# Kernel tuning notes

Hardware: AMD Instinct MI355X
Metric: run time of the kernel (lower is better)

Reference implementation:

```python
import jax, jax.numpy as jnp
import numpy as np

N_NODES = 50000
N_EDGES = 1_600_000
IN_DIM = 128
HID = 32
HEADS = 4
NEG_SLOPE = 0.2


def setup_inputs() -> dict:
    key = jax.random.key(0)
    ks = jax.random.split(key, 6)
    h = jax.random.normal(ks[0], (N_NODES, IN_DIM), dtype=jnp.float32)
    src = jax.random.randint(ks[1], (N_EDGES,), 0, N_NODES, dtype=jnp.int32)
    dst = jax.random.randint(ks[2], (N_EDGES,), 0, N_NODES, dtype=jnp.int32)
    s = 1.0 / np.sqrt(IN_DIM)  # ~ Linear default init scale
    Wq = (jax.random.normal(ks[3], (HEADS, IN_DIM, HID), dtype=jnp.float32) * s)
    Wk = (jax.random.normal(ks[4], (HEADS, IN_DIM, HID), dtype=jnp.float32) * s)
    Wv = (jax.random.normal(ks[5], (HEADS, IN_DIM, HID), dtype=jnp.float32) * s)
    return {"h": h, "src": src, "dst": dst, "Wq": Wq, "Wk": Wk, "Wv": Wv}


def _gat_forward(h, src, dst, Wq, Wk, Wv):
    n = h.shape[0]
    # per-head projections: [H, N, D]
    q = jnp.einsum('ni,hio->hno', h, Wq)
    k = jnp.einsum('ni,hio->hno', h, Wk)
    v = jnp.einsum('ni,hio->hno', h, Wv)
    # edge scores: e = leaky_relu(<q_src, k_dst>)  -> [H, E]
    e = jax.nn.leaky_relu(jnp.einsum('hed,hed->he', q[:, src], k[:, dst]),
                          negative_slope=NEG_SLOPE)
    # segment softmax over incoming edges of each dst node
    seg_max = jax.vmap(lambda x: jax.ops.segment_max(x, dst, num_segments=n))(e)
    seg_max = jax.lax.stop_gradient(jnp.where(jnp.isfinite(seg_max), seg_max, 0.0))
    ex = jnp.exp(e - seg_max[:, dst])                       # [H, E]
    denom = jax.vmap(lambda x: jax.ops.segment_sum(x, dst, num_segments=n))(ex)
    alpha = ex / jnp.maximum(denom, 1e-9)[:, dst]           # [H, E]
    # weighted scatter-sum of source values into dst nodes: [H, N, D]
    msg = alpha[..., None] * v[:, src]
    out = jax.vmap(lambda m: jax.ops.segment_sum(m, dst, num_segments=n))(msg)
    # concat heads along feature dim -> [N, H*D]
    return out.transpose(1, 0, 2).reshape(n, HEADS * HID)


def reference(h, src, dst, Wq, Wk, Wv):
    return _gat_forward(h, src, dst, Wq, Wk, Wv)
```

## Files before the change

kernel.cpp:

```cpp
#include <hip/hip_runtime.h>
#include <hip/hip_fp16.h>

#define IN_DIM 128
#define HID 32
#define HEADS 4
#define OUTC (HEADS*HID)
#define NEG_SLOPE 0.2f
#define BSH 4
#define BN 16
#define BCAP 768
#define NBMAX 3200
#define NCOLS 384
#define WPB 192

typedef _Float16 f16x8 __attribute__((ext_vector_type(8)));
typedef float    f32x4 __attribute__((ext_vector_type(4)));

__device__ __forceinline__ unsigned short f2h(float f) {
    return __half_as_ushort(__float2half_rn(f));
}
__device__ __forceinline__ float2 h2f2(unsigned u) {
    __half2 h = *reinterpret_cast<__half2*>(&u);
    return __half22float2(h);
}
__device__ __forceinline__ float qdot2(const uint2& w, const float4& kd) {
    float2 a = h2f2(w.x);
    float2 b = h2f2(w.y);
    return a.x * kd.x + a.y * kd.y + b.x * kd.z + b.y * kd.w;
}
__device__ __forceinline__ void vacc2(const uint2& w, float e, float4& acc) {
    float2 a = h2f2(w.x);
    float2 b = h2f2(w.y);
    acc.x = fmaf(e, a.x, acc.x);
    acc.y = fmaf(e, a.y, acc.y);
    acc.z = fmaf(e, b.x, acc.z);
    acc.w = fmaf(e, b.y, acc.w);
}

__global__ __launch_bounds__(256) void w_prep(
    const float* __restrict__ Wq, const float* __restrict__ Wk,
    const float* __restrict__ Wv, unsigned short* __restrict__ Wt,
    int* __restrict__ gcount)
{
    int idx = blockIdx.x * 256 + threadIdx.x;
    if (idx < NBMAX) gcount[idx] = 0;
    if (idx >= NCOLS * IN_DIM) return;
    int c = idx >> 7, k = idx & 127;
    int sel = c >> 7;
    int cc  = c & 127;
    int head = cc >> 5, dcol = cc & 31;
    const float* W = (sel == 0) ? Wk : (sel == 1) ? Wq : Wv;
    Wt[idx] = f2h(W[(size_t)head * IN_DIM * HID + (size_t)k * HID + dcol]);
}

__global__ __launch_bounds__(256) void bin_proj(
    const int* __restrict__ src, const int* __restrict__ dst,
    int* __restrict__ gcount, unsigned* __restrict__ pairs,
    const float* __restrict__ h, const unsigned short* __restrict__ Wt,
    unsigned short* __restrict__ K, unsigned short* __restrict__ Qa,
    unsigned short* __restrict__ Va,
    int ne, int nbuck, int binblk, int n)
{
    __shared__ __align__(16) char smem_raw[2 * NBMAX * 4];
    const int tid = threadIdx.x;

    if ((int)blockIdx.x < binblk) {
        int* hist = (int*)smem_raw;
        int* base = hist + NBMAX;
        const int bblk = blockIdx.x;

        for (int i = tid; i < nbuck; i += 256) hist[i] = 0;
        __syncthreads();

        const int ne4 = ne >> 2;
        const int4* s4 = (const int4*)src;
        const int4* d4 = (const int4*)dst;

        int4 sv[4], dv[4];
        int loc[16], bk[16];
        bool val[4];
#pragma unroll
        for (int k2 = 0; k2 < 4; ++k2) {
            int idx = bblk * 1024 + k2 * 256 + tid;
            val[k2] = idx < ne4;
            if (val[k2]) { sv[k2] = s4[idx]; dv[k2] = d4[idx]; }
            else { sv[k2] = make_int4(0,0,0,0); dv[k2] = make_int4(0,0,0,0); }
        }
#pragma unroll
        for (int k2 = 0; k2 < 4; ++k2) {
            int dd[4] = { dv[k2].x, dv[k2].y, dv[k2].z, dv[k2].w };
#pragma unroll
            for (int j = 0; j < 4; ++j) {
                int b = dd[j] >> BSH;
                bk[k2*4+j]  = b;
                loc[k2*4+j] = val[k2] ? atomicAdd(&hist[b], 1) : 0;
            }
        }
        __syncthreads();
        for (int i = tid; i < nbuck; i += 256)
            base[i] = hist[i] ? atomicAdd(&gcount[i], hist[i]) : 0;
        __syncthreads();
#pragma unroll
        for (int k2 = 0; k2 < 4; ++k2) {
            if (!val[k2]) continue;
            int ss[4] = { sv[k2].x, sv[k2].y, sv[k2].z, sv[k2].w };
            int dd[4] = { dv[k2].x, dv[k2].y, dv[k2].z, dv[k2].w };
#pragma unroll
            for (int j = 0; j < 4; ++j) {
                int b = bk[k2*4+j];
                int p = base[b] + loc[k2*4+j];
                if (p < BCAP)
                    pairs[(size_t)b * BCAP + p] =
                        ((unsigned)ss[j] << BSH) | (unsigned)(dd[j] & (BN-1));
            }
        }
        if (bblk == 0 && tid == 0) {
            for (int e = ne4 * 4; e < ne; ++e) {
                int b = dst[e] >> BSH;
                int p = atomicAdd(&gcount[b], 1);
                if (p < BCAP)
                    pairs[(size_t)b * BCAP + p] =
                        ((unsigned)src[e] << BSH) | (unsigned)(dst[e] & (BN-1));
            }
        }
        return;
    }

    unsigned short* hsm = (unsigned short*)smem_raw;
    const int row0 = (blockIdx.x - binblk) * 32;

    for (int idx = tid; idx < 32 * 64; idx += 256) {
        int r  = idx >> 6;
        int c2 = idx & 63;
        int gr = row0 + r;
        float2 hv = (gr < n) ? ((const float2*)h)[(size_t)gr * 64 + c2]
                             : make_float2(0.f, 0.f);
        int col = c2 * 2;
        int sc  = col ^ ((r & 7) << 3);
        __half2 packed = __floats2half2_rn(hv.x, hv.y);
        *(unsigned*)&hsm[r * IN_DIM + sc] = *(unsigned*)&packed;
    }
    __syncthreads();

    const int w = tid >> 6;
    const int l = tid & 63;
    const int l15 = l & 15;
    const int kg  = l >> 4;
    const _Float16* Wt16 = (const _Float16*)Wt;

    f32x4 acc[2][6];
#pragma unroll
    for (int rt = 0; rt < 2; ++rt)
#pragma unroll
        for (int ct = 0; ct < 6; ++ct) acc[rt][ct] = (f32x4){0.f, 0.f, 0.f, 0.f};

#pragma unroll
    for (int s = 0; s < 4; ++s) {
        int scol = (s * 32 + kg * 8) ^ ((l & 7) << 3);
        f16x8 a0 = *(const f16x8*)&hsm[l15 * IN_DIM + scol];
        f16x8 a1 = *(const f16x8*)&hsm[(l15 + 16) * IN_DIM + scol];
#pragma unroll
        for (int ct = 0; ct < 6; ++ct) {
            int c = w * 96 + ct * 16 + l15;
            f16x8 b = *(const f16x8*)&Wt16[(size_t)c * IN_DIM + s * 32 + kg * 8];
            acc[0][ct] = __builtin_amdgcn_mfma_f32_16x16x32_f16(a0, b, acc[0][ct], 0, 0, 0);
            acc[1][ct] = __builtin_amdgcn_mfma_f32_16x16x32_f16(a1, b, acc[1][ct], 0, 0, 0);
        }
    }

#pragma unroll
    for (int rt = 0; rt < 2; ++rt) {
#pragma unroll
        for (int ct = 0; ct < 6; ++ct) {
            int cD = w * 96 + ct * 16 + l15;
#pragma unroll
            for (int r = 0; r < 4; ++r) {
                int node = row0 + rt * 16 + kg * 4 + r;
                if (node >= n) continue;
                unsigned short hv = f2h(acc[rt][ct][r]);
                if (cD < 128) {
                    K[(size_t)node * OUTC + cD] = hv;
                } else if (cD < 256) {
                    Qa[(size_t)node * OUTC + (cD - 128)] = hv;
                } else {
                    Va[(size_t)node * OUTC + (cD - 256)] = hv;
                }
            }
        }
    }
}

__global__ __launch_bounds__(256) void gat_bucket(
    const unsigned* __restrict__ pairs, const int* __restrict__ gcount,
    const uint2* __restrict__ Q2, const uint2* __restrict__ V2,
    const ushort4* __restrict__ K4,
    float* __restrict__ out, int n, int nbuck)
{
    __shared__ unsigned short sl[BCAP];
    __shared__ float exls[BCAP * 4];
    __shared__ int cl[BN], cur[BN], off[BN + 1];

    const int b = blockIdx.x;
    if (b >= nbuck) return;
    const int tid = threadIdx.x;

    if (tid < BN) cl[tid] = 0;
    __syncthreads();

    int m = gcount[b]; if (m > BCAP) m = BCAP;
    const unsigned* pb = pairs + (size_t)b * BCAP;

    for (int i = tid; i < m; i += 256) atomicAdd(&cl[pb[i] & (BN - 1)], 1);
    __syncthreads();
    if (tid == 0) {
        int a = 0;
#pragma unroll
        for (int i = 0; i < BN; ++i) { off[i] = a; cur[i] = a; a += cl[i]; }
        off[BN] = a;
    }
    __syncthreads();
    for (int i = tid; i < m; i += 256) {
        unsigned p = pb[i];
        int pos = atomicAdd(&cur[p & (BN - 1)], 1);
        sl[pos] = (unsigned short)(p >> BSH);
    }
    __syncthreads();

    const int gi   = tid >> 5;
    const int l32  = tid & 31;
    const int hsel = l32 >> 3;
    const bool wr  = (l32 & 7) == 0;

    float dsum[BN / 8];

#pragma unroll
    for (int q = 0; q < BN / 8; ++q) {
        int nl   = q * 8 + gi;
        int node = b * BN + nl;
        float ds = 0.f;
        if (node < n) {
            ushort4 kh = K4[(size_t)node * 32 + l32];
            float2 k01 = h2f2(*(unsigned*)&kh.x);
            float2 k23 = h2f2(*(unsigned*)&kh.z);
            const float4 kd = make_float4(k01.x, k01.y, k23.x, k23.y);

            int j        = off[nl];
            const int je = off[nl + 1];
            for (; j + 3 < je; j += 4) {
                int s0 = sl[j], s1 = sl[j + 1], s2 = sl[j + 2], s3 = sl[j + 3];
                uint2 w0 = Q2[(size_t)s0 * 32 + l32];
                uint2 w1 = Q2[(size_t)s1 * 32 + l32];
                uint2 w2 = Q2[(size_t)s2 * 32 + l32];
                uint2 w3 = Q2[(size_t)s3 * 32 + l32];
                float p0 = qdot2(w0, kd), p1 = qdot2(w1, kd);
                float p2 = qdot2(w2, kd), p3 = qdot2(w3, kd);
#pragma unroll
                for (int o = 1; o < 8; o <<= 1) {
                    p0 += __shfl_xor(p0, o, 8);
                    p1 += __shfl_xor(p1, o, 8);
                    p2 += __shfl_xor(p2, o, 8);
                    p3 += __shfl_xor(p3, o, 8);
                }
                float e0 = __expf(p0 > 0.f ? p0 : NEG_SLOPE * p0);
                float e1 = __expf(p1 > 0.f ? p1 : NEG_SLOPE * p1);
                float e2 = __expf(p2 > 0.f ? p2 : NEG_SLOPE * p2);
                float e3 = __expf(p3 > 0.f ? p3 : NEG_SLOPE * p3);
                ds += (e0 + e1) + (e2 + e3);
                if (wr) {
                    exls[(j    ) * 4 + hsel] = e0;
                    exls[(j + 1) * 4 + hsel] = e1;
                    exls[(j + 2) * 4 + hsel] = e2;
                    exls[(j + 3) * 4 + hsel] = e3;
                }
            }
            for (; j < je; ++j) {
                int s0 = sl[j];
                uint2 w0 = Q2[(size_t)s0 * 32 + l32];
                float p0 = qdot2(w0, kd);
#pragma unroll
                for (int o = 1; o < 8; o <<= 1) p0 += __shfl_xor(p0, o, 8);
                float e0 = __expf(p0 > 0.f ? p0 : NEG_SLOPE * p0);
                ds += e0;
                if (wr) exls[j * 4 + hsel] = e0;
            }
        }
        dsum[q] = ds;
    }
    __syncthreads();

#pragma unroll
    for (int q = 0; q < BN / 8; ++q) {
        int nl   = q * 8 + gi;
        int node = b * BN + nl;
        if (node >= n) continue;

        int j        = off[nl];
        const int je = off[nl + 1];
        float4 acc = make_float4(0.f, 0.f, 0.f, 0.f);

        for (; j + 3 < je; j += 4) {
            int s0 = sl[j], s1 = sl[j + 1], s2 = sl[j + 2], s3 = sl[j + 3];
            uint2 w0 = V2[(size_t)s0 * 32 + l32];
            uint2 w1 = V2[(size_t)s1 * 32 + l32];
            uint2 w2 = V2[(size_t)s2 * 32 + l32];
            uint2 w3 = V2[(size_t)s3 * 32 + l32];
            float e0 = exls[(j    ) * 4 + hsel];
            float e1 = exls[(j + 1) * 4 + hsel];
            float e2 = exls[(j + 2) * 4 + hsel];
            float e3 = exls[(j + 3) * 4 + hsel];
            vacc2(w0, e0, acc); vacc2(w1, e1, acc);
            vacc2(w2, e2, acc); vacc2(w3, e3, acc);
        }
        for (; j < je; ++j) {
            int s0 = sl[j];
            uint2 w0 = V2[(size_t)s0 * 32 + l32];
            float e0 = exls[j * 4 + hsel];
            vacc2(w0, e0, acc);
        }

        float inv = 1.f / fmaxf(dsum[q], 1e-9f);
        float4 o; o.x = acc.x*inv; o.y = acc.y*inv; o.z = acc.z*inv; o.w = acc.w*inv;
        ((float4*)out)[(size_t)node * 32 + l32] = o;
    }
}

extern "C" void kernel_launch(void* const* d_in, const int* in_sizes, int n_in,
                              void* d_out, int out_size, void* d_ws, size_t ws_size,
                              hipStream_t stream) {
    const float* h   = (const float*)d_in[0];
    const int*   src = (const int*)d_in[1];
    const int*   dst = (const int*)d_in[2];
    const float* Wq  = (const float*)d_in[3];
    const float* Wk  = (const float*)d_in[4];
    const float* Wv  = (const float*)d_in[5];
    float* out = (float*)d_out;

    const int n     = in_sizes[0] / IN_DIM;
    const int ne    = in_sizes[1];
    const int nbuck = (n + BN - 1) >> BSH;

    unsigned short* K      = (unsigned short*)d_ws;
    unsigned short* Qa     = K  + (size_t)n * OUTC;
    unsigned short* Va     = Qa + (size_t)n * OUTC;
    int*            gcount = (int*)(Va + (size_t)n * OUTC);
    unsigned*       pairs  = (unsigned*)(gcount + NBMAX);
    unsigned short* Wt     = (unsigned short*)(pairs + (size_t)NBMAX * BCAP);

    w_prep<<<WPB, 256, 0, stream>>>(Wq, Wk, Wv, Wt, gcount);

    int ne4     = ne >> 2;
    int binblk  = (ne4 + 1023) / 1024;
    int projblk = (n + 31) / 32;
    bin_proj<<<binblk + projblk, 256, 0, stream>>>(
        src, dst, gcount, pairs, h, Wt, K, Qa, Va, ne, nbuck, binblk, n);

    gat_bucket<<<nbuck, 256, 0, stream>>>(pairs, gcount, (const uint2*)Qa,
                                          (const uint2*)Va, (const ushort4*)K,
                                          out, n, nbuck);
}
```

Before: 171.6 us.

## Split edge binning into two-pass radix partition by coarse then fine bucket

Replaces the single-pass binning, which kept a 3200-entry shared histogram and scattered into 3125 buckets, with two passes. The first pass partitions edges into 25 coarse partitions using a small shared histogram and packs src and dst into one word. A new pass2 kernel then splits each partition into 128 fine buckets, with the aim of making scatter writes and global atomics more local. This costs an extra kernel launch and an extra read and write of all edge pairs. The 16-bit packing assumes node ids stay below 65536.

After: 171.0 us. No clear change (-0.4%).

```diff
diff --git a/kernel.cpp b/kernel.cpp
--- a/kernel.cpp
+++ b/kernel.cpp
@@ -12,6 +12,10 @@
 #define NBMAX 3200
 #define NCOLS 384
 #define WPB 192
+#define NP 25
+#define PSH 11
+#define PCAP 72704
+#define PBLK 18
 
 typedef _Float16 f16x8 __attribute__((ext_vector_type(8)));
 typedef float    f32x4 __attribute__((ext_vector_type(4)));
@@ -40,10 +44,11 @@
 __global__ __launch_bounds__(256) void w_prep(
     const float* __restrict__ Wq, const float* __restrict__ Wk,
     const float* __restrict__ Wv, unsigned short* __restrict__ Wt,
-    int* __restrict__ gcount)
+    int* __restrict__ gcount, int* __restrict__ pcount)
 {
     int idx = blockIdx.x * 256 + threadIdx.x;
     if (idx < NBMAX) gcount[idx] = 0;
+    if (idx >= NBMAX && idx < NBMAX + NP) pcount[idx - NBMAX] = 0;
     if (idx >= NCOLS * IN_DIM) return;
     int c = idx >> 7, k = idx & 127;
     int sel = c >> 7;
@@ -53,23 +58,23 @@
     Wt[idx] = f2h(W[(size_t)head * IN_DIM * HID + (size_t)k * HID + dcol]);
 }
 
-__global__ __launch_bounds__(256) void bin_proj(
+__global__ __launch_bounds__(256) void part_proj(
     const int* __restrict__ src, const int* __restrict__ dst,
-    int* __restrict__ gcount, unsigned* __restrict__ pairs,
+    int* __restrict__ pcount, unsigned* __restrict__ ppairs,
     const float* __restrict__ h, const unsigned short* __restrict__ Wt,
     unsigned short* __restrict__ K, unsigned short* __restrict__ Qa,
     unsigned short* __restrict__ Va,
-    int ne, int nbuck, int binblk, int n)
+    int ne, int binblk, int n)
 {
-    __shared__ __align__(16) char smem_raw[2 * NBMAX * 4];
+    __shared__ __align__(16) char smem_raw[32 * IN_DIM * 2];
     const int tid = threadIdx.x;
 
     if ((int)blockIdx.x < binblk) {
         int* hist = (int*)smem_raw;
-        int* base = hist + NBMAX;
+        int* base = hist + 32;
         const int bblk = blockIdx.x;
 
-        for (int i = tid; i < nbuck; i += 256) hist[i] = 0;
+        if (tid < 32) hist[tid] = 0;
         __syncthreads();
 
         const int ne4 = ne >> 2;
@@ -77,7 +82,7 @@
         const int4* d4 = (const int4*)dst;
 
         int4 sv[4], dv[4];
-        int loc[16], bk[16];
+        int loc[16], pk[16];
         bool val[4];
 #pragma unroll
         for (int k2 = 0; k2 < 4; ++k2) {
@@ -91,14 +96,13 @@
             int dd[4] = { dv[k2].x, dv[k2].y, dv[k2].z, dv[k2].w };
 #pragma unroll
             for (int j = 0; j < 4; ++j) {
-                int b = dd[j] >> BSH;
-                bk[k2*4+j]  = b;
-                loc[k2*4+j] = val[k2] ? atomicAdd(&hist[b], 1) : 0;
+                int p = dd[j] >> PSH;
+                pk[k2*4+j]  = p;
+                loc[k2*4+j] = val[k2] ? atomicAdd(&hist[p], 1) : 0;
             }
         }
         __syncthreads();
-        for (int i = tid; i < nbuck; i += 256)
-            base[i] = hist[i] ? atomicAdd(&gcount[i], hist[i]) : 0;
+        if (tid < 32) base[tid] = hist[tid] ? atomicAdd(&pcount[tid], hist[tid]) : 0;
         __syncthreads();
 #pragma unroll
         for (int k2 = 0; k2 < 4; ++k2) {
@@ -107,20 +111,20 @@
             int dd[4] = { dv[k2].x, dv[k2].y, dv[k2].z, dv[k2].w };
 #pragma unroll
             for (int j = 0; j < 4; ++j) {
-                int b = bk[k2*4+j];
-                int p = base[b] + loc[k2*4+j];
-                if (p < BCAP)
-                    pairs[(size_t)b * BCAP + p] =
-                        ((unsigned)ss[j] << BSH) | (unsigned)(dd[j] & (BN-1));
+                int p   = pk[k2*4+j];
+                int pos = base[p] + loc[k2*4+j];
+                if (pos < PCAP)
+                    ppairs[(size_t)p * PCAP + pos] =
+                        ((unsigned)ss[j] << 16) | (unsigned)dd[j];
             }
         }
         if (bblk == 0 && tid == 0) {
             for (int e = ne4 * 4; e < ne; ++e) {
-                int b = dst[e] >> BSH;
-                int p = atomicAdd(&gcount[b], 1);
-                if (p < BCAP)
-                    pairs[(size_t)b * BCAP + p] =
-                        ((unsigned)src[e] << BSH) | (unsigned)(dst[e] & (BN-1));
+                int p   = dst[e] >> PSH;
+                int pos = atomicAdd(&pcount[p], 1);
+                if (pos < PCAP)
+                    ppairs[(size_t)p * PCAP + pos] =
+                        ((unsigned)src[e] << 16) | (unsigned)dst[e];
             }
         }
         return;
@@ -187,6 +191,54 @@
                 }
             }
         }
+    }
+}
+
+__global__ __launch_bounds__(256) void pass2(
+    const unsigned* __restrict__ ppairs, const int* __restrict__ pcount,
+    int* __restrict__ gcount, unsigned* __restrict__ pairs)
+{
+    __shared__ int hist[128], base[128];
+    const int p   = blockIdx.x / PBLK;
+    const int c   = blockIdx.x % PBLK;
+    const int tid = threadIdx.x;
+
+    int mp = pcount[p]; if (mp > PCAP) mp = PCAP;
+    const int i0 = c * 4096;
+    if (i0 >= mp) return;
+    const int iend = min(i0 + 4096, mp);
+
+    if (tid < 128) hist[tid] = 0;
+    __syncthreads();
+
+    const unsigned* pp = ppairs + (size_t)p * PCAP;
+    unsigned rec[16];
+    int loc[16], lb[16];
+#pragma unroll
+    for (int k = 0; k < 16; ++k) {
+        int i = i0 + k * 256 + tid;
+        if (i < iend) {
+            unsigned r = pp[i];
+            rec[k] = r;
+            int b = ((r & 0xFFFFu) >> BSH) & 127;
+            lb[k]  = b;
+            loc[k] = atomicAdd(&hist[b], 1);
+        } else {
+            rec[k] = 0; lb[k] = -1; loc[k] = 0;
+        }
+    }
+    __syncthreads();
+    if (tid < 128) base[tid] = hist[tid] ? atomicAdd(&gcount[p * 128 + tid], hist[tid]) : 0;
+    __syncthreads();
+#pragma unroll
+    for (int k = 0; k < 16; ++k) {
+        if (lb[k] < 0) continue;
+        unsigned r = rec[k];
+        int gb  = p * 128 + lb[k];
+        int pos = base[lb[k]] + loc[k];
+        if (pos < BCAP)
+            pairs[(size_t)gb * BCAP + pos] =
+                ((r >> 16) << BSH) | (r & (BN - 1));
     }
 }
 
@@ -343,16 +395,20 @@
     unsigned short* Qa     = K  + (size_t)n * OUTC;
     unsigned short* Va     = Qa + (size_t)n * OUTC;
     int*            gcount = (int*)(Va + (size_t)n * OUTC);
-    unsigned*       pairs  = (unsigned*)(gcount + NBMAX);
+    int*            pcount = gcount + NBMAX;
+    unsigned*       ppairs = (unsigned*)(pcount + 64);
+    unsigned*       pairs  = ppairs + (size_t)NP * PCAP;
     unsigned short* Wt     = (unsigned short*)(pairs + (size_t)NBMAX * BCAP);
 
-    w_prep<<<WPB, 256, 0, stream>>>(Wq, Wk, Wv, Wt, gcount);
+    w_prep<<<WPB, 256, 0, stream>>>(Wq, Wk, Wv, Wt, gcount, pcount);
 
     int ne4     = ne >> 2;
     int binblk  = (ne4 + 1023) / 1024;
     int projblk = (n + 31) / 32;
-    bin_proj<<<binblk + projblk, 256, 0, stream>>>(
-        src, dst, gcount, pairs, h, Wt, K, Qa, Va, ne, nbuck, binblk, n);
+    part_proj<<<binblk + projblk, 256, 0, stream>>>(
+        src, dst, pcount, ppairs, h, Wt, K, Qa, Va, ne, binblk, n);
+
+    pass2<<<NP * PBLK, 256, 0, stream>>>(ppairs, pcount, gcount, pairs);
 
     gat_bucket<<<nbuck, 256, 0, stream>>>(pairs, gcount, (const uint2*)Qa,
                                           (const uint2*)Va, (const ushort4*)K,
```

## Bin edges into 128-node partitions and stage projection output through LDS

Applied to the files above, without the earlier changes.

Edge binning now uses 391 coarse partitions of 128 destination nodes instead of 3125 buckets of 16. This cuts shared-memory histogram size and the number of global atomics, and makes pair writes less scattered. Each gat_bucket block now scans its whole partition (about 4096 pairs) and filters for its 16-node sub-bucket, so it reads roughly 8x more pair data. The projection path also loads h as float4 and stages the fp16 outputs in LDS, so global K/Q/V stores are 8-byte vectors instead of scattered 2-byte writes.

Measured after the change: 173.3 us. No clear change (+1.0%).

```diff
diff --git a/kernel.cpp b/kernel.cpp
--- a/kernel.cpp
+++ b/kernel.cpp
@@ -6,12 +6,13 @@
 #define HEADS 4
 #define OUTC (HEADS*HID)
 #define NEG_SLOPE 0.2f
-#define BSH 4
 #define BN 16
 #define BCAP 768
-#define NBMAX 3200
+#define NPMAX 512
+#define PCAP 4864
 #define NCOLS 384
 #define WPB 192
+#define OSTRIDE 392
 
 typedef _Float16 f16x8 __attribute__((ext_vector_type(8)));
 typedef float    f32x4 __attribute__((ext_vector_type(4)));
@@ -40,10 +41,10 @@
 __global__ __launch_bounds__(256) void w_prep(
     const float* __restrict__ Wq, const float* __restrict__ Wk,
     const float* __restrict__ Wv, unsigned short* __restrict__ Wt,
-    int* __restrict__ gcount)
+    int* __restrict__ pcount)
 {
     int idx = blockIdx.x * 256 + threadIdx.x;
-    if (idx < NBMAX) gcount[idx] = 0;
+    if (idx < NPMAX) pcount[idx] = 0;
     if (idx >= NCOLS * IN_DIM) return;
     int c = idx >> 7, k = idx & 127;
     int sel = c >> 7;
@@ -53,23 +54,23 @@
     Wt[idx] = f2h(W[(size_t)head * IN_DIM * HID + (size_t)k * HID + dcol]);
 }
 
-__global__ __launch_bounds__(256) void bin_proj(
+__global__ __launch_bounds__(256) void part_proj(
     const int* __restrict__ src, const int* __restrict__ dst,
-    int* __restrict__ gcount, unsigned* __restrict__ pairs,
+    int* __restrict__ pcount, unsigned* __restrict__ ppairs,
     const float* __restrict__ h, const unsigned short* __restrict__ Wt,
     unsigned short* __restrict__ K, unsigned short* __restrict__ Qa,
     unsigned short* __restrict__ Va,
-    int ne, int nbuck, int binblk, int n)
+    int ne, int binblk, int n, int npart)
 {
-    __shared__ __align__(16) char smem_raw[2 * NBMAX * 4];
+    __shared__ __align__(16) char smem_raw[32 * OSTRIDE * 2];
     const int tid = threadIdx.x;
 
     if ((int)blockIdx.x < binblk) {
         int* hist = (int*)smem_raw;
-        int* base = hist + NBMAX;
+        int* base = hist + NPMAX;
         const int bblk = blockIdx.x;
 
-        for (int i = tid; i < nbuck; i += 256) hist[i] = 0;
+        for (int i = tid; i < npart; i += 256) hist[i] = 0;
         __syncthreads();
 
         const int ne4 = ne >> 2;
@@ -77,7 +78,7 @@
         const int4* d4 = (const int4*)dst;
 
         int4 sv[4], dv[4];
-        int loc[16], bk[16];
+        int loc[16], pk[16];
         bool val[4];
 #pragma unroll
         for (int k2 = 0; k2 < 4; ++k2) {
@@ -91,14 +92,14 @@
             int dd[4] = { dv[k2].x, dv[k2].y, dv[k2].z, dv[k2].w };
 #pragma unroll
             for (int j = 0; j < 4; ++j) {
-                int b = dd[j] >> BSH;
-                bk[k2*4+j]  = b;
-                loc[k2*4+j] = val[k2] ? atomicAdd(&hist[b], 1) : 0;
+                int p = dd[j] >> 7;
+                pk[k2*4+j]  = p;
+                loc[k2*4+j] = val[k2] ? atomicAdd(&hist[p], 1) : 0;
             }
         }
         __syncthreads();
-        for (int i = tid; i < nbuck; i += 256)
-            base[i] = hist[i] ? atomicAdd(&gcount[i], hist[i]) : 0;
+        for (int i = tid; i < npart; i += 256)
+            base[i] = hist[i] ? atomicAdd(&pcount[i], hist[i]) : 0;
         __syncthreads();
 #pragma unroll
         for (int k2 = 0; k2 < 4; ++k2) {
@@ -107,20 +108,20 @@
             int dd[4] = { dv[k2].x, dv[k2].y, dv[k2].z, dv[k2].w };
 #pragma unroll
             for (int j = 0; j < 4; ++j) {
-                int b = bk[k2*4+j];
-                int p = base[b] + loc[k2*4+j];
-                if (p < BCAP)
-                    pairs[(size_t)b * BCAP + p] =
-                        ((unsigned)ss[j] << BSH) | (unsigned)(dd[j] & (BN-1));
+                int p   = pk[k2*4+j];
+                int pos = base[p] + loc[k2*4+j];
+                if (pos < PCAP)
+                    ppairs[(size_t)p * PCAP + pos] =
+                        ((unsigned)ss[j] << 7) | (unsigned)(dd[j] & 127);
             }
         }
         if (bblk == 0 && tid == 0) {
             for (int e = ne4 * 4; e < ne; ++e) {
-                int b = dst[e] >> BSH;
-                int p = atomicAdd(&gcount[b], 1);
-                if (p < BCAP)
-                    pairs[(size_t)b * BCAP + p] =
-                        ((unsigned)src[e] << BSH) | (unsigned)(dst[e] & (BN-1));
+                int p   = dst[e] >> 7;
+                int pos = atomicAdd(&pcount[p], 1);
+                if (pos < PCAP)
+                    ppairs[(size_t)p * PCAP + pos] =
+                        ((unsigned)src[e] << 7) | (unsigned)(dst[e] & 127);
             }
         }
         return;
@@ -129,16 +130,19 @@
     unsigned short* hsm = (unsigned short*)smem_raw;
     const int row0 = (blockIdx.x - binblk) * 32;
 
-    for (int idx = tid; idx < 32 * 64; idx += 256) {
-        int r  = idx >> 6;
-        int c2 = idx & 63;
+    for (int idx = tid; idx < 32 * 32; idx += 256) {
+        int r  = idx >> 5;
+        int c4 = idx & 31;
         int gr = row0 + r;
-        float2 hv = (gr < n) ? ((const float2*)h)[(size_t)gr * 64 + c2]
-                             : make_float2(0.f, 0.f);
-        int col = c2 * 2;
-        int sc  = col ^ ((r & 7) << 3);
-        __half2 packed = __floats2half2_rn(hv.x, hv.y);
-        *(unsigned*)&hsm[r * IN_DIM + sc] = *(unsigned*)&packed;
+        float4 hv = (gr < n) ? ((const float4*)h)[(size_t)gr * 32 + c4]
+                             : make_float4(0.f, 0.f, 0.f, 0.f);
+        int sc = (c4 * 4) ^ ((r & 7) << 3);
+        __half2 p01 = __floats2half2_rn(hv.x, hv.y);
+        __half2 p23 = __floats2half2_rn(hv.z, hv.w);
+        uint2 u;
+        u.x = *(unsigned*)&p01;
+        u.y = *(unsigned*)&p23;
+        *(uint2*)&hsm[r * IN_DIM + sc] = u;
     }
     __syncthreads();
 
@@ -167,7 +171,9 @@
             acc[1][ct] = __builtin_amdgcn_mfma_f32_16x16x32_f16(a1, b, acc[1][ct], 0, 0, 0);
         }
     }
-
+    __syncthreads();
+
+    unsigned short* osm = (unsigned short*)smem_raw;
 #pragma unroll
     for (int rt = 0; rt < 2; ++rt) {
 #pragma unroll
@@ -175,42 +181,54 @@
             int cD = w * 96 + ct * 16 + l15;
 #pragma unroll
             for (int r = 0; r < 4; ++r) {
-                int node = row0 + rt * 16 + kg * 4 + r;
-                if (node >= n) continue;
-                unsigned short hv = f2h(acc[rt][ct][r]);
-                if (cD < 128) {
-                    K[(size_t)node * OUTC + cD] = hv;
-                } else if (cD < 256) {
-                    Qa[(size_t)node * OUTC + (cD - 128)] = hv;
-                } else {
-                    Va[(size_t)node * OUTC + (cD - 256)] = hv;
-                }
-            }
-        }
+                int rowl = rt * 16 + kg * 4 + r;
+                osm[rowl * OSTRIDE + cD] = f2h(acc[rt][ct][r]);
+            }
+        }
+    }
+    __syncthreads();
+
+    for (int c = tid; c < 32 * 96; c += 256) {
+        int row  = c / 96;
+        int col4 = c - row * 96;
+        int node = row0 + row;
+        if (node >= n) continue;
+        uint2 v = *(const uint2*)&osm[row * OSTRIDE + col4 * 4];
+        int colbase = col4 * 4;
+        if (colbase < 128)
+            *(uint2*)&K [(size_t)node * OUTC + colbase] = v;
+        else if (colbase < 256)
+            *(uint2*)&Qa[(size_t)node * OUTC + (colbase - 128)] = v;
+        else
+            *(uint2*)&Va[(size_t)node * OUTC + (colbase - 256)] = v;
     }
 }
 
 __global__ __launch_bounds__(256) void gat_bucket(
-    const unsigned* __restrict__ pairs, const int* __restrict__ gcount,
+    const unsigned* __restrict__ ppairs, const int* __restrict__ pcount,
     const uint2* __restrict__ Q2, const uint2* __restrict__ V2,
     const ushort4* __restrict__ K4,
-    float* __restrict__ out, int n, int nbuck)
+    float* __restrict__ out, int n)
 {
     __shared__ unsigned short sl[BCAP];
     __shared__ float exls[BCAP * 4];
     __shared__ int cl[BN], cur[BN], off[BN + 1];
 
-    const int b = blockIdx.x;
-    if (b >= nbuck) return;
+    const int b   = blockIdx.x;
+    const int p   = b >> 3;
+    const int sub = b & 7;
     const int tid = threadIdx.x;
 
     if (tid < BN) cl[tid] = 0;
     __syncthreads();
 
-    int m = gcount[b]; if (m > BCAP) m = BCAP;
-    const unsigned* pb = pairs + (size_t)b * BCAP;
-
-    for (int i = tid; i < m; i += 256) atomicAdd(&cl[pb[i] & (BN - 1)], 1);
+    int m = pcount[p]; if (m > PCAP) m = PCAP;
+    const unsigned* pp = ppairs + (size_t)p * PCAP;
+
+    for (int i = tid; i < m; i += 256) {
+        unsigned r = pp[i];
+        if (((r >> 4) & 7) == (unsigned)sub) atomicAdd(&cl[r & (BN - 1)], 1);
+    }
     __syncthreads();
     if (tid == 0) {
         int a = 0;
@@ -220,9 +238,11 @@
     }
     __syncthreads();
     for (int i = tid; i < m; i += 256) {
-        unsigned p = pb[i];
-        int pos = atomicAdd(&cur[p & (BN - 1)], 1);
-        sl[pos] = (unsigned short)(p >> BSH);
+        unsigned r = pp[i];
+        if (((r >> 4) & 7) == (unsigned)sub) {
+            int pos = atomicAdd(&cur[r & (BN - 1)], 1);
+            if (pos < BCAP) sl[pos] = (unsigned short)(r >> 7);
+        }
     }
     __syncthreads();
 
@@ -244,8 +264,8 @@
             float2 k23 = h2f2(*(unsigned*)&kh.z);
             const float4 kd = make_float4(k01.x, k01.y, k23.x, k23.y);
 
-            int j        = off[nl];
-            const int je = off[nl + 1];
+            int j        = min(off[nl], BCAP);
+            const int je = min(off[nl + 1], BCAP);
             for (; j + 3 < je; j += 4) {
                 int s0 = sl[j], s1 = sl[j + 1], s2 = sl[j + 2], s3 = sl[j + 3];
                 uint2 w0 = Q2[(size_t)s0 * 32 + l32];
@@ -294,8 +314,8 @@
         int node = b * BN + nl;
         if (node >= n) continue;
 
-        int j        = off[nl];
-        const int je = off[nl + 1];
+        int j        = min(off[nl], BCAP);
+        const int je = min(off[nl + 1], BCAP);
         float4 acc = make_float4(0.f, 0.f, 0.f, 0.f);
 
         for (; j + 3 < je; j += 4) {
@@ -337,24 +357,25 @@
 
     const int n     = in_sizes[0] / IN_DIM;
     const int ne    = in_sizes[1];
-    const int nbuck = (n + BN - 1) >> BSH;
+    const int nbuck = (n + BN - 1) / BN;
+    const int npart = (n + 127) >> 7;
 
     unsigned short* K      = (unsigned short*)d_ws;
     unsigned short* Qa     = K  + (size_t)n * OUTC;
     unsigned short* Va     = Qa + (size_t)n * OUTC;
-    int*            gcount = (int*)(Va + (size_t)n * OUTC);
-    unsigned*       pairs  = (unsigned*)(gcount + NBMAX);
-    unsigned short* Wt     = (unsigned short*)(pairs + (size_t)NBMAX * BCAP);
-
-    w_prep<<<WPB, 256, 0, stream>>>(Wq, Wk, Wv, Wt, gcount);
+    int*            pcount = (int*)(Va + (size_t)n * OUTC);
+    unsigned*       ppairs = (unsigned*)(pcount + NPMAX);
+    unsigned short* Wt     = (unsigned short*)(ppairs + (size_t)NPMAX * PCAP);
+
+    w_prep<<<WPB, 256, 0, stream>>>(Wq, Wk, Wv, Wt, pcount);
 
     int ne4     = ne >> 2;
     int binblk  = (ne4 + 1023) / 1024;
     int projblk = (n + 31) / 32;
-    bin_proj<<<binblk + projblk, 256, 0, stream>>>(
-        src, dst, gcount, pairs, h, Wt, K, Qa, Va, ne, nbuck, binblk, n);
-
-    gat_bucket<<<nbuck, 256, 0, stream>>>(pairs, gcount, (const uint2*)Qa,
+    part_proj<<<binblk + projblk, 256, 0, stream>>>(
+        src, dst, pcount, ppairs, h, Wt, K, Qa, Va, ne, binblk, n, npart);
+
+    gat_bucket<<<nbuck, 256, 0, stream>>>(ppairs, pcount, (const uint2*)Qa,
                                           (const uint2*)Va, (const ushort4*)K,
-                                          out, n, nbuck);
-}
+                                          out, n);
+}
```
